# Optimization experiments

Hardware: AMD Instinct MI355X
Metric: run time of the kernel (lower is better)

## Reference

```python
import jax, jax.numpy as jnp
import numpy as np

DIM = 768
HEADS = 12
HEAD_DIM = DIM // HEADS
SCALE = HEAD_DIM ** -0.5


def setup_inputs() -> dict:
    key = jax.random.key(0)
    k1, k2, k3, k4, k5 = jax.random.split(key, 5)
    x = jax.random.normal(k1, (8, 1024, DIM), dtype=jnp.float32)
    # torch Linear default init ~ U(-1/sqrt(fan_in), 1/sqrt(fan_in)); scale similarly
    s = 1.0 / np.sqrt(DIM)
    qkv_w = jax.random.uniform(k2, (3 * DIM, DIM), minval=-s, maxval=s, dtype=jnp.float32)
    qkv_b = jax.random.uniform(k3, (3 * DIM,), minval=-s, maxval=s, dtype=jnp.float32)
    proj_w = jax.random.uniform(k4, (DIM, DIM), minval=-s, maxval=s, dtype=jnp.float32)
    proj_b = jax.random.uniform(k5, (DIM,), minval=-s, maxval=s, dtype=jnp.float32)
    return {"x": x, "qkv_w": qkv_w, "qkv_b": qkv_b, "proj_w": proj_w, "proj_b": proj_b}


def reference(x, qkv_w, qkv_b, proj_w, proj_b):
    B, N, C = x.shape
    qkv = x @ qkv_w.T + qkv_b                      # [B, N, 3C]
    qkv = qkv.reshape(B, N, 3, HEADS, HEAD_DIM)
    q = jnp.transpose(qkv[:, :, 0], (0, 2, 1, 3))  # [B, H, N, D]
    k = jnp.transpose(qkv[:, :, 1], (0, 2, 1, 3))
    v = jnp.transpose(qkv[:, :, 2], (0, 2, 1, 3))
    attn = jnp.einsum('bhnd,bhmd->bhnm', q, k) * SCALE  # [B, H, N, N]
    attn = jax.nn.softmax(attn, axis=-1)
    out = jnp.einsum('bhnm,bhmd->bhnd', attn, v)   # [B, H, N, D]
    out = jnp.transpose(out, (0, 2, 1, 3)).reshape(B, N, C)
    return out @ proj_w.T + proj_b
```

## Files before the change

kernel.cpp:

```cpp
#include <hip/hip_runtime.h>
#include <stdint.h>

typedef unsigned short ushort_t;
typedef __attribute__((ext_vector_type(8))) short short8;
typedef __attribute__((ext_vector_type(4))) float f32x4;
typedef __attribute__((address_space(1))) uint32_t as1_u32;
typedef __attribute__((address_space(3))) uint32_t as3_u32;

#define MFMA16(a, b, c) __builtin_amdgcn_mfma_f32_16x16x32_bf16(a, b, c, 0, 0, 0)

#define PIPE_BAR4() asm volatile("s_waitcnt vmcnt(4)\n\ts_barrier" ::: "memory")
#define PIPE_BAR6() asm volatile("s_waitcnt vmcnt(6)\n\ts_barrier" ::: "memory")
#define PIPE_BAR0() asm volatile("s_waitcnt vmcnt(0)\n\ts_barrier" ::: "memory")
#define BAR_RAW()   asm volatile("s_barrier" ::: "memory")

__device__ __forceinline__ void cp16(const void* g, void* l) {
    __builtin_amdgcn_global_load_lds((as1_u32*)(uintptr_t)g,
                                     (as3_u32*)(uint32_t)(uintptr_t)l, 16, 0, 0);
}

__device__ __forceinline__ ushort_t f2bf(float f) {
    uint32_t u = __float_as_uint(f);
    u += 0x7fffu + ((u >> 16) & 1u);
    return (ushort_t)(u >> 16);
}

__global__ __launch_bounds__(256) void cvt3_kernel(const float* __restrict__ x,
                                                   const float* __restrict__ w1,
                                                   const float* __restrict__ w2,
                                                   ushort_t* __restrict__ xb,
                                                   ushort_t* __restrict__ wb1,
                                                   ushort_t* __restrict__ wb2) {
    const int bid = blockIdx.x;
    const float4* src;
    ushort4* dst;
    int i;
    if (bid < 6144)      { src = (const float4*)x;  dst = (ushort4*)xb;  i = bid * 256 + threadIdx.x; }
    else if (bid < 7872) { src = (const float4*)w1; dst = (ushort4*)wb1; i = (bid - 6144) * 256 + threadIdx.x; }
    else                 { src = (const float4*)w2; dst = (ushort4*)wb2; i = (bid - 7872) * 256 + threadIdx.x; }
    float4 v = src[i];
    ushort4 o;
    o.x = f2bf(v.x); o.y = f2bf(v.y); o.z = f2bf(v.z); o.w = f2bf(v.w);
    dst[i] = o;
}

__global__ __launch_bounds__(256) void qkv_gemm(const ushort_t* __restrict__ xb,
                                                const ushort_t* __restrict__ wq,
                                                const float* __restrict__ bias,
                                                ushort_t* __restrict__ Qg,
                                                ushort_t* __restrict__ Kg,
                                                ushort_t* __restrict__ Vt) {
    __shared__ __align__(16) ushort_t smem[17408];
    const int t = threadIdx.x, w = t >> 6, lane = t & 63;
    const int m16 = lane & 15, q = lane >> 4;
    const int n0 = blockIdx.x * 128, m0 = blockIdx.y * 128;
    const int wm = w >> 1, wn = w & 1;
    ushort_t* const A0 = smem;
    ushort_t* const B0 = smem + 4096;
    ushort_t* const A1 = smem + 8192;
    ushort_t* const B1 = smem + 12288;

    f32x4 acc[4][4];
#pragma unroll
    for (int i = 0; i < 4; ++i)
#pragma unroll
        for (int j = 0; j < 4; ++j) acc[i][j] = (f32x4)0.f;

    auto issueT = [&](int kk, ushort_t* As, ushort_t* Bs) {
#pragma unroll
        for (int s = 0; s < 2; ++s) {
            const int i2 = s * 256 + t;
            const int lb = (s * 256 + w * 64) * 8;
            cp16(&xb[(m0 + (i2 >> 2)) * 768 + kk + (i2 & 3) * 8], &As[lb]);
            cp16(&wq[(n0 + (i2 >> 2)) * 768 + kk + (i2 & 3) * 8], &Bs[lb]);
        }
    };

    issueT(0, A0, B0);
    issueT(32, A1, B1);
#pragma unroll 2
    for (int kki = 0; kki < 24; ++kki) {
        if (kki < 23) { PIPE_BAR4(); } else { PIPE_BAR0(); }
        ushort_t* As = (kki & 1) ? A1 : A0;
        ushort_t* Bs = (kki & 1) ? B1 : B0;
        short8 a[4], b[4];
#pragma unroll
        for (int i = 0; i < 4; ++i) a[i] = *(const short8*)&As[(wm * 64 + i * 16 + m16) * 32 + q * 8];
#pragma unroll
        for (int j = 0; j < 4; ++j) b[j] = *(const short8*)&Bs[(wn * 64 + j * 16 + m16) * 32 + q * 8];
#pragma unroll
        for (int i = 0; i < 4; ++i)
#pragma unroll
            for (int j = 0; j < 4; ++j) acc[i][j] = MFMA16(a[i], b[j], acc[i][j]);
        BAR_RAW();
        if (kki < 22) issueT((kki + 2) * 32, As, Bs);
    }

    const int three = n0 / 768;
    const int b_idx = m0 >> 10;

    if (three < 2) {
        ushort_t* dst = three ? Kg : Qg;
        const float scale = three ? 1.0f : 0.18033688011112042f;
#pragma unroll
        for (int j = 0; j < 4; ++j) {
            float bj = bias[n0 + wn * 64 + j * 16 + m16];
#pragma unroll
            for (int i = 0; i < 4; ++i)
#pragma unroll
                for (int r = 0; r < 4; ++r)
                    smem[(wm * 64 + i * 16 + q * 4 + r) * 136 + wn * 64 + j * 16 + m16] =
                        f2bf((acc[i][j][r] + bj) * scale);
        }
        __syncthreads();
        const int col0 = n0 - three * 768;
#pragma unroll
        for (int u8 = 0; u8 < 8; ++u8) {
            int u = u8 * 256 + t;
            int row = u >> 4, cg = u & 15;
            uint4 vv = *(const uint4*)&smem[row * 136 + cg * 8];
            int col = col0 + cg * 8;
            int hh = col >> 6, dd = col & 63;
            int n = (m0 & 1023) + row;
            *(uint4*)&dst[((b_idx * 12 + hh) * 1024 + n) * 64 + dd] = vv;
        }
    } else {
        const int nq_base = (m0 & 1023) + wm * 64;
#pragma unroll
        for (int j = 0; j < 4; ++j) {
            int col = n0 + wn * 64 + j * 16 + m16 - 1536;
            float bj = bias[col + 1536];
            int hh = col >> 6, dd = col & 63;
            ushort_t* base = Vt + ((b_idx * 12 + hh) * 64 + dd) * 1024;
#pragma unroll
            for (int i = 0; i < 4; ++i) {
                ushort4 pk;
                pk.x = f2bf(acc[i][j][0] + bj);
                pk.y = f2bf(acc[i][j][1] + bj);
                pk.z = f2bf(acc[i][j][2] + bj);
                pk.w = f2bf(acc[i][j][3] + bj);
                *(ushort4*)&base[nq_base + i * 16 + q * 4] = pk;
            }
        }
    }
}

__global__ __launch_bounds__(256) void attn_kernel(const ushort_t* __restrict__ Qg,
                                                   const ushort_t* __restrict__ Kg,
                                                   const ushort_t* __restrict__ Vt,
                                                   ushort_t* __restrict__ Og) {
    __shared__ __align__(16) ushort_t Ks[128 * 64];
    __shared__ __align__(16) ushort_t Vs[64 * 128];
    __shared__ __align__(16) ushort_t Ps[4 * 16 * 136];
    const int t = threadIdx.x, w = t >> 6, lane = t & 63;
    const int m16 = lane & 15, q = lane >> 4;
    const int qt = blockIdx.x, bh = blockIdx.y;
    const int b = bh / 12, h = bh % 12;
    const ushort_t* Qbh = Qg + bh * 65536;
    const ushort_t* Kbh = Kg + bh * 65536;
    const ushort_t* Vbh = Vt + bh * 65536;
    ushort_t* Pw = &Ps[w * 2176];

    const int q0 = qt * 128 + w * 32;
    short8 qf[2][2];
#pragma unroll
    for (int i = 0; i < 2; ++i)
#pragma unroll
        for (int kd = 0; kd < 2; ++kd)
            qf[i][kd] = *(const short8*)&Qbh[(q0 + i * 16 + m16) * 64 + kd * 32 + q * 8];

    f32x4 o[2][4];
#pragma unroll
    for (int i = 0; i < 2; ++i)
#pragma unroll
        for (int ds = 0; ds < 4; ++ds) o[i][ds] = (f32x4)0.f;
    float l_run[2] = {0.f, 0.f};

    for (int kt = 0; kt < 8; ++kt) {
        const int key0 = kt * 128;
#pragma unroll
        for (int p = 0; p < 4; ++p) {
            const int c = p * 256 + t;
            const int lbase = (p * 256 + w * 64) * 8;
            { int key = c >> 3, g = c & 7;
              cp16(&Kbh[(key0 + key) * 64 + ((g ^ (key & 7)) * 8)], &Ks[lbase]); }
            { int d = c >> 4, g2 = c & 15;
              cp16(&Vbh[d * 1024 + key0 + ((g2 ^ (d & 15)) * 8)], &Vs[lbase]); }
        }
        __syncthreads();

        f32x4 st[2][8];
#pragma unroll
        for (int ks = 0; ks < 8; ++ks) {
            const ushort_t* kr = &Ks[(ks * 16 + m16) * 64];
            short8 a0 = *(const short8*)&kr[(q ^ (m16 & 7)) * 8];
            short8 a1 = *(const short8*)&kr[((4 + q) ^ (m16 & 7)) * 8];
            st[0][ks] = MFMA16(a1, qf[0][1], MFMA16(a0, qf[0][0], (f32x4)0.f));
            st[1][ks] = MFMA16(a1, qf[1][1], MFMA16(a0, qf[1][0], (f32x4)0.f));
        }

#pragma unroll
        for (int i = 0; i < 2; ++i) {
            float ps = 0.f;
#pragma unroll
            for (int ks = 0; ks < 8; ++ks) {
                float p0 = exp2f(st[i][ks][0]);
                float p1 = exp2f(st[i][ks][1]);
                float p2 = exp2f(st[i][ks][2]);
                float p3 = exp2f(st[i][ks][3]);
                ps += (p0 + p1) + (p2 + p3);
                uint32_t u0 = __float_as_uint(p0) + 0x8000u;
                uint32_t u1 = __float_as_uint(p1) + 0x8000u;
                uint32_t u2 = __float_as_uint(p2) + 0x8000u;
                uint32_t u3 = __float_as_uint(p3) + 0x8000u;
                uint2 pk;
                pk.x = __builtin_amdgcn_perm(u1, u0, 0x07060302u);
                pk.y = __builtin_amdgcn_perm(u3, u2, 0x07060302u);
                *(uint2*)&Pw[m16 * 136 + ks * 16 + q * 4] = pk;
            }
            ps += __shfl_xor(ps, 16, 64);
            ps += __shfl_xor(ps, 32, 64);
            l_run[i] += ps;
#pragma unroll
            for (int kkk = 0; kkk < 4; ++kkk) {
                short8 ap = *(const short8*)&Pw[m16 * 136 + kkk * 32 + q * 8];
#pragma unroll
                for (int ds = 0; ds < 4; ++ds) {
                    short8 vb = *(const short8*)&Vs[(ds * 16 + m16) * 128 + (((kkk * 4 + q) ^ m16) * 8)];
                    o[i][ds] = MFMA16(ap, vb, o[i][ds]);
                }
            }
        }
        __syncthreads();
    }
#pragma unroll
    for (int i = 0; i < 2; ++i) {
        float linv = 1.f / l_run[i];
#pragma unroll
        for (int r = 0; r < 4; ++r) {
            float lr = __shfl(linv, q * 4 + r, 64);
            int row = b * 1024 + q0 + i * 16 + q * 4 + r;
#pragma unroll
            for (int ds = 0; ds < 4; ++ds)
                Og[row * 768 + h * 64 + ds * 16 + m16] = f2bf(o[i][ds][r] * lr);
        }
    }
}

__global__ __launch_bounds__(128) void proj_gemm(const ushort_t* __restrict__ Ob,
                                                 const ushort_t* __restrict__ wp,
                                                 const float* __restrict__ bias,
                                                 float* __restrict__ out) {
    __shared__ __align__(16) ushort_t smem[12288];
    const int t = threadIdx.x, w = t >> 6, lane = t & 63;
    const int m16 = lane & 15, q = lane >> 4;
    const int n0 = blockIdx.x * 64, m0 = blockIdx.y * 128;
    ushort_t* const A0 = smem;
    ushort_t* const B0 = smem + 4096;
    ushort_t* const A1 = smem + 6144;
    ushort_t* const B1 = smem + 10240;

    f32x4 acc[4][4];
#pragma unroll
    for (int i = 0; i < 4; ++i)
#pragma unroll
        for (int j = 0; j < 4; ++j) acc[i][j] = (f32x4)0.f;

    auto issueT = [&](int kk, ushort_t* As, ushort_t* Bs) {
#pragma unroll
        for (int s = 0; s < 4; ++s) {
            const int c = s * 128 + t;
            cp16(&Ob[(m0 + (c >> 2)) * 768 + kk + (c & 3) * 8], &As[(s * 128 + w * 64) * 8]);
        }
#pragma unroll
        for (int s = 0; s < 2; ++s) {
            const int c = s * 128 + t;
            cp16(&wp[(n0 + (c >> 2)) * 768 + kk + (c & 3) * 8], &Bs[(s * 128 + w * 64) * 8]);
        }
    };

    issueT(0, A0, B0);
    issueT(32, A1, B1);
#pragma unroll 2
    for (int kki = 0; kki < 24; ++kki) {
        if (kki < 23) { PIPE_BAR6(); } else { PIPE_BAR0(); }
        ushort_t* As = (kki & 1) ? A1 : A0;
        ushort_t* Bs = (kki & 1) ? B1 : B0;
        short8 a[4], b[4];
#pragma unroll
        for (int i = 0; i < 4; ++i) a[i] = *(const short8*)&As[(w * 64 + i * 16 + m16) * 32 + q * 8];
#pragma unroll
        for (int j = 0; j < 4; ++j) b[j] = *(const short8*)&Bs[(j * 16 + m16) * 32 + q * 8];
#pragma unroll
        for (int i = 0; i < 4; ++i)
#pragma unroll
            for (int j = 0; j < 4; ++j) acc[i][j] = MFMA16(a[i], b[j], acc[i][j]);
        BAR_RAW();
        if (kki < 22) issueT((kki + 2) * 32, As, Bs);
    }

#pragma unroll
    for (int j = 0; j < 4; ++j) {
        int col = n0 + j * 16 + m16;
        float bj = bias[col];
#pragma unroll
        for (int i = 0; i < 4; ++i)
#pragma unroll
            for (int r = 0; r < 4; ++r) {
                int row = m0 + w * 64 + i * 16 + q * 4 + r;
                out[row * 768 + col] = acc[i][j][r] + bj;
            }
    }
}

extern "C" void kernel_launch(void* const* d_in, const int* in_sizes, int n_in,
                              void* d_out, int out_size, void* d_ws, size_t ws_size,
                              hipStream_t stream) {
    const float* x      = (const float*)d_in[0];
    const float* qkv_w  = (const float*)d_in[1];
    const float* qkv_b  = (const float*)d_in[2];
    const float* proj_w = (const float*)d_in[3];
    const float* proj_b = (const float*)d_in[4];
    float* out = (float*)d_out;

    char* ws = (char*)d_ws;
    ushort_t* xb    = (ushort_t*)(ws);
    ushort_t* wqkv  = (ushort_t*)(ws + 12582912);
    ushort_t* wproj = (ushort_t*)(ws + 16121856);
    ushort_t* Qg    = (ushort_t*)(ws + 17301504);
    ushort_t* Kg    = (ushort_t*)(ws + 29884416);
    ushort_t* Vt    = (ushort_t*)(ws + 42467328);
    ushort_t* Og    = (ushort_t*)(ws + 55050240);

    cvt3_kernel<<<8448, 256, 0, stream>>>(x, qkv_w, proj_w, xb, wqkv, wproj);
    qkv_gemm<<<dim3(18, 64), 256, 0, stream>>>(xb, wqkv, qkv_b, Qg, Kg, Vt);
    attn_kernel<<<dim3(8, 96), 256, 0, stream>>>(Qg, Kg, Vt, Og);
    proj_gemm<<<dim3(12, 64), 128, 0, stream>>>(Og, wproj, proj_b, out);
}
```

Before: 213.0 us.

## Double-buffer K tiles and reuse consumed K buffer for P in attention

The attention loop now prefetches the next K tile into a second LDS buffer while the current tile is processed. V for the next tile is issued right after the PV matmul finishes. The separate P scratch buffer is removed, and P is written into the just-consumed K buffer with an XOR swizzle, which keeps LDS usage roughly flat. This is meant to hide global-load latency behind the QK and softmax compute. In exchange it adds an extra barrier per iteration, and the V load is still only partly overlapped.

```diff
diff --git a/kernel.cpp b/kernel.cpp
--- a/kernel.cpp
+++ b/kernel.cpp
@@ -13,6 +13,7 @@
 #define PIPE_BAR6() asm volatile("s_waitcnt vmcnt(6)\n\ts_barrier" ::: "memory")
 #define PIPE_BAR0() asm volatile("s_waitcnt vmcnt(0)\n\ts_barrier" ::: "memory")
 #define BAR_RAW()   asm volatile("s_barrier" ::: "memory")
+#define SCHED_FENCE() __builtin_amdgcn_sched_barrier(0)
 
 __device__ __forceinline__ void cp16(const void* g, void* l) {
     __builtin_amdgcn_global_load_lds((as1_u32*)(uintptr_t)g,
@@ -149,9 +150,8 @@
                                                    const ushort_t* __restrict__ Kg,
                                                    const ushort_t* __restrict__ Vt,
                                                    ushort_t* __restrict__ Og) {
-    __shared__ __align__(16) ushort_t Ks[128 * 64];
+    __shared__ __align__(16) ushort_t Ks[2][128 * 64];
     __shared__ __align__(16) ushort_t Vs[64 * 128];
-    __shared__ __align__(16) ushort_t Ps[4 * 16 * 136];
     const int t = threadIdx.x, w = t >> 6, lane = t & 63;
     const int m16 = lane & 15, q = lane >> 4;
     const int qt = blockIdx.x, bh = blockIdx.y;
@@ -159,7 +159,6 @@
     const ushort_t* Qbh = Qg + bh * 65536;
     const ushort_t* Kbh = Kg + bh * 65536;
     const ushort_t* Vbh = Vt + bh * 65536;
-    ushort_t* Pw = &Ps[w * 2176];
 
     const int q0 = qt * 128 + w * 32;
     short8 qf[2][2];
@@ -176,29 +175,45 @@
         for (int ds = 0; ds < 4; ++ds) o[i][ds] = (f32x4)0.f;
     float l_run[2] = {0.f, 0.f};
 
-    for (int kt = 0; kt < 8; ++kt) {
-        const int key0 = kt * 128;
+    auto issueK = [&](int key0, ushort_t* dstbuf) {
 #pragma unroll
         for (int p = 0; p < 4; ++p) {
             const int c = p * 256 + t;
-            const int lbase = (p * 256 + w * 64) * 8;
-            { int key = c >> 3, g = c & 7;
-              cp16(&Kbh[(key0 + key) * 64 + ((g ^ (key & 7)) * 8)], &Ks[lbase]); }
-            { int d = c >> 4, g2 = c & 15;
-              cp16(&Vbh[d * 1024 + key0 + ((g2 ^ (d & 15)) * 8)], &Vs[lbase]); }
-        }
-        __syncthreads();
+            int key = c >> 3, g = c & 7;
+            cp16(&Kbh[(key0 + key) * 64 + ((g ^ (key & 7)) * 8)], &dstbuf[(p * 256 + w * 64) * 8]);
+        }
+    };
+    auto issueV = [&](int key0) {
+#pragma unroll
+        for (int p = 0; p < 4; ++p) {
+            const int c = p * 256 + t;
+            int d = c >> 4, g2 = c & 15;
+            cp16(&Vbh[d * 1024 + key0 + ((g2 ^ (d & 15)) * 8)], &Vs[(p * 256 + w * 64) * 8]);
+        }
+    };
+
+    issueK(0, Ks[0]);
+    issueV(0);
+
+#pragma unroll 2
+    for (int kt = 0; kt < 8; ++kt) {
+        PIPE_BAR0();
+        ushort_t* Kcur = Ks[kt & 1];
+        if (kt < 7) issueK((kt + 1) * 128, Ks[(kt + 1) & 1]);
 
         f32x4 st[2][8];
 #pragma unroll
         for (int ks = 0; ks < 8; ++ks) {
-            const ushort_t* kr = &Ks[(ks * 16 + m16) * 64];
+            const ushort_t* kr = &Kcur[(ks * 16 + m16) * 64];
             short8 a0 = *(const short8*)&kr[(q ^ (m16 & 7)) * 8];
             short8 a1 = *(const short8*)&kr[((4 + q) ^ (m16 & 7)) * 8];
             st[0][ks] = MFMA16(a1, qf[0][1], MFMA16(a0, qf[0][0], (f32x4)0.f));
             st[1][ks] = MFMA16(a1, qf[1][1], MFMA16(a0, qf[1][0], (f32x4)0.f));
         }
-
+        SCHED_FENCE();
+        BAR_RAW();
+
+        ushort_t* Pw = &Kcur[w * 2048];
 #pragma unroll
         for (int i = 0; i < 2; ++i) {
             float ps = 0.f;
@@ -216,14 +231,14 @@
                 uint2 pk;
                 pk.x = __builtin_amdgcn_perm(u1, u0, 0x07060302u);
                 pk.y = __builtin_amdgcn_perm(u3, u2, 0x07060302u);
-                *(uint2*)&Pw[m16 * 136 + ks * 16 + q * 4] = pk;
+                *(uint2*)&Pw[m16 * 128 + (((2 * ks + (q >> 1)) ^ m16) * 8) + (q & 1) * 4] = pk;
             }
             ps += __shfl_xor(ps, 16, 64);
             ps += __shfl_xor(ps, 32, 64);
             l_run[i] += ps;
 #pragma unroll
             for (int kkk = 0; kkk < 4; ++kkk) {
-                short8 ap = *(const short8*)&Pw[m16 * 136 + kkk * 32 + q * 8];
+                short8 ap = *(const short8*)&Pw[m16 * 128 + (((kkk * 4 + q) ^ m16) * 8)];
 #pragma unroll
                 for (int ds = 0; ds < 4; ++ds) {
                     short8 vb = *(const short8*)&Vs[(ds * 16 + m16) * 128 + (((kkk * 4 + q) ^ m16) * 8)];
@@ -231,7 +246,9 @@
                 }
             }
         }
-        __syncthreads();
+        SCHED_FENCE();
+        BAR_RAW();
+        if (kt < 7) issueV((kt + 1) * 128);
     }
 #pragma unroll
     for (int i = 0; i < 2; ++i) {
```

After: 235.0 us. 1.1x slower.
